# Performance work log

Hardware: AMD Instinct MI355X
Metric: run time of the kernel (lower is better)

The kernel has to match this reference:

```python
import jax, jax.numpy as jnp
import numpy as np
import math

D_MODEL = 1024
D_STATE = 16
D_CONV = 4
EXPAND = 2
D_INNER = EXPAND * D_MODEL
DT_RANK = math.ceil(D_MODEL / 16)
EPS = 1e-5


def setup_inputs() -> dict:
    key = jax.random.key(0)
    ks = jax.random.split(key, 8)
    B, L = 2, 1024
    s = 0.02
    return {
        "hidden_states": jax.random.normal(ks[0], (B, L, D_MODEL), jnp.float32),
        "norm_weight": jnp.ones((D_MODEL,), jnp.float32),
        "in_proj_w": (jax.random.normal(ks[1], (2 * D_INNER, D_MODEL), jnp.float32) * s),
        "conv_w": (jax.random.normal(ks[2], (D_INNER, D_CONV), jnp.float32) * s),
        "conv_b": jnp.zeros((D_INNER,), jnp.float32),
        "x_proj_w": (jax.random.normal(ks[3], (DT_RANK + 2 * D_STATE, D_INNER), jnp.float32) * s),
        "dt_proj_w": (jax.random.normal(ks[4], (D_INNER, DT_RANK), jnp.float32) * s),
        "dt_proj_b": jax.random.uniform(ks[5], (D_INNER,), jnp.float32, -4.0, -2.0),
        "A_log": jnp.log(jnp.broadcast_to(jnp.arange(1, D_STATE + 1, dtype=jnp.float32), (D_INNER, D_STATE))),
        "D": jnp.ones((D_INNER,), jnp.float32),
        "out_proj_w": (jax.random.normal(ks[6], (D_MODEL, D_INNER), jnp.float32) * s),
    }


def _rmsnorm(x, w):
    # Faithful to source: rms = ||x||_2 / sqrt(d); x / (rms + eps) * w
    norm = jnp.linalg.norm(x, axis=-1, keepdims=True)
    rms = norm * (1.0 / math.sqrt(x.shape[-1]))
    return w * (x / (rms + EPS))


def _mamba(h, in_proj_w, conv_w, conv_b, x_proj_w, dt_proj_w, dt_proj_b, A_log, D, out_proj_w):
    B, L, _ = h.shape
    xz = h @ in_proj_w.T                      # (B,L,2*D_INNER)
    x, z = jnp.split(xz, 2, axis=-1)          # each (B,L,D_INNER)

    # causal depthwise conv1d along L, kernel D_CONV
    xpad = jnp.pad(x, ((0, 0), (D_CONV - 1, 0), (0, 0)))
    xc = conv_b
    for k in range(D_CONV):                   # tiny fixed loop over kernel taps
        xc = xc + xpad[:, k:k + L, :] * conv_w[:, k]
    xc = jax.nn.silu(xc)                      # (B,L,D_INNER)

    x_dbl = xc @ x_proj_w.T                   # (B,L,DT_RANK+2N)
    dt, Bm, Cm = jnp.split(x_dbl, [DT_RANK, DT_RANK + D_STATE], axis=-1)
    dt = jax.nn.softplus(dt @ dt_proj_w.T + dt_proj_b)   # (B,L,D_INNER)

    A = -jnp.exp(A_log)                       # (D_INNER,N)
    deltaA = jnp.exp(dt[..., None] * A)                      # (B,L,D_INNER,N)
    deltaBu = (dt * xc)[..., None] * Bm[:, :, None, :]        # (B,L,D_INNER,N)

    def step(hst, inp):
        dA, dBu, Ct = inp
        hst = dA * hst + dBu                  # (B,D_INNER,N)
        y = jnp.einsum('bdn,bn->bd', hst, Ct)
        return hst, y

    h0 = jnp.zeros((B, D_INNER, D_STATE), xc.dtype)
    _, ys = jax.lax.scan(step, h0, (deltaA.swapaxes(0, 1), deltaBu.swapaxes(0, 1), Cm.swapaxes(0, 1)))
    y = ys.swapaxes(0, 1)                     # (B,L,D_INNER)
    y = y + D * xc
    y = y * jax.nn.silu(z)
    return y @ out_proj_w.T                   # (B,L,D_MODEL)


def reference(hidden_states, norm_weight, in_proj_w, conv_w, conv_b, x_proj_w,
              dt_proj_w, dt_proj_b, A_log, D, out_proj_w):
    residual = hidden_states
    h = _rmsnorm(residual, norm_weight)
    out = _mamba(h, in_proj_w, conv_w, conv_b, x_proj_w, dt_proj_w, dt_proj_b,
                 A_log, D, out_proj_w)
    return out, residual
```

## Files before the change

### kernel.cpp

```cpp
#include <hip/hip_runtime.h>

typedef __bf16 bf16x8 __attribute__((ext_vector_type(8)));
typedef float f32x4 __attribute__((ext_vector_type(4)));

__device__ __forceinline__ float b2f(ushort u) {
    union { unsigned int i; float f; } v;
    v.i = ((unsigned int)u) << 16;
    return v.f;
}
__device__ __forceinline__ ushort f2b(float f) {
    union { float f; unsigned int i; } v;
    v.f = f;
    unsigned int x = v.i;
    unsigned int r = (x + 0x7fffu + ((x >> 16) & 1u)) >> 16;
    return (ushort)r;
}
__device__ __forceinline__ float fexp2(float x) {
#if __has_builtin(__builtin_amdgcn_exp2f)
    return __builtin_amdgcn_exp2f(x);
#else
    return exp2f(x);
#endif
}
__device__ __forceinline__ void gload16(const ushort* g, ushort* l) {
    __builtin_amdgcn_global_load_lds(
        (const __attribute__((address_space(1))) unsigned int*)g,
        (__attribute__((address_space(3))) unsigned int*)l, 16, 0, 0);
}
__device__ __forceinline__ bf16x8 ldsfrag(const ushort* s, int row, int cq) {
    int p = cq ^ (row & 7);
    return *(const bf16x8*)(s + row * 64 + p * 8);
}

#define D_MODEL 1024
#define D_INNER 2048
#define D_STATE 16
#define DT_RANK 64
#define NTOK    2048
#define LSEQ    1024
#define NCH     32
#define LC      32
#define KSL     16
#define LOG2E   1.44269504088896f

__global__ __launch_bounds__(256) void prep_kernel(
    const float* __restrict__ hs, const float* __restrict__ w,
    ushort* __restrict__ hout, float* __restrict__ resid,
    const float* __restrict__ inproj, const float* __restrict__ outproj,
    const float* __restrict__ xprojw, const float* __restrict__ dtw,
    ushort* __restrict__ wIn, ushort* __restrict__ wOut,
    ushort* __restrict__ xpw, ushort* __restrict__ dtwb,
    float* __restrict__ xdbl, float* __restrict__ outz)
{
    int blk = blockIdx.x;
    int tid = threadIdx.x;
    if (blk < NTOK) {
        int t = blk;
        float4 r4 = *(const float4*)(hs + (size_t)t * D_MODEL + tid * 4);
        float s = r4.x * r4.x + r4.y * r4.y + r4.z * r4.z + r4.w * r4.w;
        #pragma unroll
        for (int off = 32; off >= 1; off >>= 1) s += __shfl_xor(s, off);
        __shared__ float red[4];
        int lane = tid & 63, wid = tid >> 6;
        if (lane == 0) red[wid] = s;
        __syncthreads();
        float tot = red[0] + red[1] + red[2] + red[3];
        float inv = 1.0f / (sqrtf(tot) * (1.0f / 32.0f) + 1e-5f);
        float4 w4 = *(const float4*)(w + tid * 4);
        ushort4 o;
        o.x = f2b(w4.x * r4.x * inv);
        o.y = f2b(w4.y * r4.y * inv);
        o.z = f2b(w4.z * r4.z * inv);
        o.w = f2b(w4.w * r4.w * inv);
        *(ushort4*)(hout + (size_t)t * D_MODEL + tid * 4) = o;
        *(float4*)(resid + (size_t)t * D_MODEL + tid * 4) = r4;
    } else if (blk < NTOK + 6464) {
        int i = (blk - NTOK) * 256 + tid;
        const float* src; ushort* dst; int off;
        if (i < 1048576)      { src = inproj;  dst = wIn;  off = i; }
        else if (i < 1572864) { src = outproj; dst = wOut; off = i - 1048576; }
        else if (i < 1622016) { src = xprojw;  dst = xpw;  off = i - 1572864; }
        else if (i < 1654784) { src = dtw;     dst = dtwb; off = i - 1622016; }
        else return;
        float4 v = *(const float4*)(src + (size_t)off * 4);
        ushort4 o;
        o.x = f2b(v.x); o.y = f2b(v.y); o.z = f2b(v.z); o.w = f2b(v.w);
        *(ushort4*)(dst + (size_t)off * 4) = o;
    } else if (blk < NTOK + 6464 + 192) {
        int i = (blk - NTOK - 6464) * 256 + tid;
        if (i < 49152)
            *(float4*)(xdbl + (size_t)i * 4) = (float4){0.f, 0.f, 0.f, 0.f};
    } else {
        int i = (blk - NTOK - 6464 - 192) * 256 + tid;
        if (i < 524288)
            *(float4*)(outz + (size_t)i * 4) = (float4){0.f, 0.f, 0.f, 0.f};
    }
}

__global__ __launch_bounds__(256) void gemm_xz_kernel(
    const ushort* __restrict__ Ag, const ushort* __restrict__ Wg,
    ushort* __restrict__ xq, ushort* __restrict__ zq, int K)
{
    __shared__ __align__(16) ushort sA[128 * 64];
    __shared__ __align__(16) ushort sB[128 * 64];
    int tid = threadIdx.x;
    int bm = blockIdx.x, bn = blockIdx.y;
    int wid = tid >> 6, lane = tid & 63;
    int wm = (wid >> 1) * 64, wn = (wid & 1) * 64;
    int l16 = lane & 15, q = lane >> 4;

    f32x4 acc[4][4];
    #pragma unroll
    for (int i = 0; i < 4; i++)
        #pragma unroll
        for (int j = 0; j < 4; j++)
            acc[i][j] = (f32x4){0.f, 0.f, 0.f, 0.f};

    const ushort* Abase = Ag + (size_t)bm * 128 * K;
    const ushort* Wbase = Wg + (size_t)bn * 128 * K;

    int segr = lane >> 3, segc = lane & 7;
    size_t goff[4]; int sseg[4];
    #pragma unroll
    for (int t = 0; t < 4; t++) {
        int s = wid * 4 + t;
        int r = s * 8 + segr;
        int gc = segc ^ (r & 7);
        sseg[t] = s * 512;
        goff[t] = (size_t)r * K + gc * 8;
    }

    for (int k0 = 0; k0 < K; k0 += 64) {
        __syncthreads();
        #pragma unroll
        for (int t = 0; t < 4; t++) {
            gload16(Abase + goff[t] + k0, sA + sseg[t]);
            gload16(Wbase + goff[t] + k0, sB + sseg[t]);
        }
        __syncthreads();
        #pragma unroll
        for (int ks = 0; ks < 2; ks++) {
            int cq = ks * 4 + q;
            bf16x8 af[4], bfr[4];
            #pragma unroll
            for (int i = 0; i < 4; i++)
                af[i] = ldsfrag(sA, wm + i * 16 + l16, cq);
            #pragma unroll
            for (int j = 0; j < 4; j++)
                bfr[j] = ldsfrag(sB, wn + j * 16 + l16, cq);
            #pragma unroll
            for (int i = 0; i < 4; i++)
                #pragma unroll
                for (int j = 0; j < 4; j++)
                    acc[i][j] = __builtin_amdgcn_mfma_f32_16x16x32_bf16(af[i], bfr[j], acc[i][j], 0, 0, 0);
        }
    }

    ushort* dst = (bn < 16) ? xq : zq;
    int row0 = bm * 128 + wm + q * 4;
    int col0 = (bn & 15) * 128 + wn + l16;
    #pragma unroll
    for (int i = 0; i < 4; i++)
        #pragma unroll
        for (int j = 0; j < 4; j++)
            #pragma unroll
            for (int r = 0; r < 4; r++)
                dst[(size_t)(row0 + i * 16 + r) * D_INNER + col0 + j * 16] =
                    f2b(acc[i][j][r]);
}

__global__ __launch_bounds__(256) void gemm_out_kernel(
    const ushort* __restrict__ Ag, const ushort* __restrict__ Wg,
    float* __restrict__ Cf)
{
    __shared__ __align__(16) ushort sA[128 * 64];
    __shared__ __align__(16) ushort sB[128 * 64];
    const int K = D_INNER;
    int tid = threadIdx.x;
    int bm = blockIdx.x, bn = blockIdx.y, bz = blockIdx.z;
    int wid = tid >> 6, lane = tid & 63;
    int wm = (wid >> 1) * 64, wn = (wid & 1) * 64;
    int l16 = lane & 15, q = lane >> 4;

    f32x4 acc[4][4];
    #pragma unroll
    for (int i = 0; i < 4; i++)
        #pragma unroll
        for (int j = 0; j < 4; j++)
            acc[i][j] = (f32x4){0.f, 0.f, 0.f, 0.f};

    const ushort* Abase = Ag + (size_t)bm * 128 * K;
    const ushort* Wbase = Wg + (size_t)bn * 128 * K;

    int segr = lane >> 3, segc = lane & 7;
    size_t goff[4]; int sseg[4];
    #pragma unroll
    for (int t = 0; t < 4; t++) {
        int s = wid * 4 + t;
        int r = s * 8 + segr;
        int gc = segc ^ (r & 7);
        sseg[t] = s * 512;
        goff[t] = (size_t)r * K + gc * 8;
    }

    int kbeg = bz * (K / 2), kend = kbeg + K / 2;
    for (int k0 = kbeg; k0 < kend; k0 += 64) {
        __syncthreads();
        #pragma unroll
        for (int t = 0; t < 4; t++) {
            gload16(Abase + goff[t] + k0, sA + sseg[t]);
            gload16(Wbase + goff[t] + k0, sB + sseg[t]);
        }
        __syncthreads();
        #pragma unroll
        for (int ks = 0; ks < 2; ks++) {
            int cq = ks * 4 + q;
            bf16x8 af[4], bfr[4];
            #pragma unroll
            for (int i = 0; i < 4; i++)
                af[i] = ldsfrag(sA, wm + i * 16 + l16, cq);
            #pragma unroll
            for (int j = 0; j < 4; j++)
                bfr[j] = ldsfrag(sB, wn + j * 16 + l16, cq);
            #pragma unroll
            for (int i = 0; i < 4; i++)
                #pragma unroll
                for (int j = 0; j < 4; j++)
                    acc[i][j] = __builtin_amdgcn_mfma_f32_16x16x32_bf16(af[i], bfr[j], acc[i][j], 0, 0, 0);
        }
    }

    int row0 = bm * 128 + wm + q * 4;
    int col0 = bn * 128 + wn + l16;
    #pragma unroll
    for (int i = 0; i < 4; i++)
        #pragma unroll
        for (int j = 0; j < 4; j++)
            #pragma unroll
            for (int r = 0; r < 4; r++)
                atomicAdd(&Cf[(size_t)(row0 + i * 16 + r) * D_MODEL + col0 + j * 16],
                          acc[i][j][r]);
}

__global__ __launch_bounds__(256) void conv_silu_kernel(
    const ushort* __restrict__ xq, const float* __restrict__ cw,
    const float* __restrict__ cb, ushort* __restrict__ xcb)
{
    int t = blockIdx.x;
    int d0 = threadIdx.x * 8;
    int l = t & (LSEQ - 1), b = t >> 10;

    ushort v[4][8];
    bool has[4];
    #pragma unroll
    for (int k = 0; k < 4; k++) {
        int ll = l - 3 + k;
        has[k] = (ll >= 0);
        if (has[k])
            *(uint4*)v[k] = *(const uint4*)(xq + (((size_t)(b * LSEQ + ll)) << 11) + d0);
    }
    ushort o[8];
    #pragma unroll
    for (int j = 0; j < 8; j++) {
        float4 w4 = *(const float4*)(cw + (size_t)(d0 + j) * 4);
        float wk[4] = {w4.x, w4.y, w4.z, w4.w};
        float acc = cb[d0 + j];
        #pragma unroll
        for (int k = 0; k < 4; k++)
            if (has[k]) acc += b2f(v[k][j]) * wk[k];
        o[j] = f2b(acc / (1.f + __expf(-acc)));
    }
    *(uint4*)(xcb + (((size_t)t) << 11) + d0) = *(const uint4*)o;
}

__global__ __launch_bounds__(256) void xproj_partial_kernel(
    const ushort* __restrict__ xcb, const ushort* __restrict__ wq,
    float* __restrict__ xdbl)
{
    __shared__ __align__(16) ushort sA[128 * 40];
    __shared__ __align__(16) ushort sB[96 * 40];
    int tid = threadIdx.x;
    int bm = blockIdx.x, sl = blockIdx.y;
    int wid = tid >> 6, lane = tid & 63;
    int wm = wid * 32;
    int l16 = lane & 15, q = lane >> 4;

    f32x4 acc[2][6];
    #pragma unroll
    for (int i = 0; i < 2; i++)
        #pragma unroll
        for (int j = 0; j < 6; j++)
            acc[i][j] = (f32x4){0.f, 0.f, 0.f, 0.f};

    const ushort* Abase = xcb + (size_t)bm * 128 * D_INNER;
    int kbase = sl * (D_INNER / KSL);

    for (int kk = 0; kk < D_INNER / KSL; kk += 32) {
        int k0 = kbase + kk;
        __syncthreads();
        #pragma unroll
        for (int i = tid; i < 512; i += 256) {
            int r = i >> 2, c = (i & 3) << 3;
            *(uint4*)(sA + r * 40 + c) = *(const uint4*)(Abase + (size_t)r * D_INNER + k0 + c);
        }
        for (int i = tid; i < 384; i += 256) {
            int r = i >> 2, c = (i & 3) << 3;
            *(uint4*)(sB + r * 40 + c) = *(const uint4*)(wq + (size_t)r * D_INNER + k0 + c);
        }
        __syncthreads();
        bf16x8 af[2], bfr[6];
        #pragma unroll
        for (int i = 0; i < 2; i++)
            af[i] = *(const bf16x8*)(sA + (wm + i * 16 + l16) * 40 + q * 8);
        #pragma unroll
        for (int j = 0; j < 6; j++)
            bfr[j] = *(const bf16x8*)(sB + (j * 16 + l16) * 40 + q * 8);
        #pragma unroll
        for (int i = 0; i < 2; i++)
            #pragma unroll
            for (int j = 0; j < 6; j++)
                acc[i][j] = __builtin_amdgcn_mfma_f32_16x16x32_bf16(af[i], bfr[j], acc[i][j], 0, 0, 0);
    }

    int row0 = bm * 128 + wm + q * 4;
    #pragma unroll
    for (int i = 0; i < 2; i++)
        #pragma unroll
        for (int j = 0; j < 6; j++)
            #pragma unroll
            for (int r = 0; r < 4; r++)
                atomicAdd(&xdbl[(size_t)(row0 + i * 16 + r) * 96 + j * 16 + l16],
                          acc[i][j][r]);
}

__global__ __launch_bounds__(256) void dt_gemm_kernel(
    const float* __restrict__ xdbl, const ushort* __restrict__ dtwq,
    const float* __restrict__ dtb, ushort* __restrict__ dtout)
{
    __shared__ __align__(16) ushort sA[64 * 72];
    __shared__ __align__(16) ushort sB[64 * 72];
    int tid = threadIdx.x;
    int bm = blockIdx.x, bn = blockIdx.y;
    int wid = tid >> 6, lane = tid & 63;
    int wm = wid * 16;
    int l16 = lane & 15, q = lane >> 4;

    const float* Abase = xdbl + (size_t)bm * 64 * 96;
    const ushort* Bbase = dtwq + (size_t)bn * 64 * DT_RANK;
    #pragma unroll
    for (int i = tid; i < 512; i += 256) {
        int r = i >> 3, c = (i & 7) << 3;
        float4 v0 = *(const float4*)(Abase + (size_t)r * 96 + c);
        float4 v1 = *(const float4*)(Abase + (size_t)r * 96 + c + 4);
        ushort o[8] = {f2b(v0.x), f2b(v0.y), f2b(v0.z), f2b(v0.w),
                       f2b(v1.x), f2b(v1.y), f2b(v1.z), f2b(v1.w)};
        *(uint4*)(sA + r * 72 + c) = *(const uint4*)o;
        *(uint4*)(sB + r * 72 + c) = *(const uint4*)(Bbase + (size_t)r * DT_RANK + c);
    }
    __syncthreads();

    f32x4 acc[4];
    #pragma unroll
    for (int j = 0; j < 4; j++) acc[j] = (f32x4){0.f, 0.f, 0.f, 0.f};

    #pragma unroll
    for (int ks = 0; ks < 2; ks++) {
        bf16x8 af = *(const bf16x8*)(sA + (wm + l16) * 72 + ks * 32 + q * 8);
        bf16x8 bfr[4];
        #pragma unroll
        for (int j = 0; j < 4; j++)
            bfr[j] = *(const bf16x8*)(sB + (j * 16 + l16) * 72 + ks * 32 + q * 8);
        #pragma unroll
        for (int j = 0; j < 4; j++)
            acc[j] = __builtin_amdgcn_mfma_f32_16x16x32_bf16(af, bfr[j], acc[j], 0, 0, 0);
    }

    __syncthreads();
    #pragma unroll
    for (int j = 0; j < 4; j++) {
        float bias = dtb[bn * 64 + j * 16 + l16];
        #pragma unroll
        for (int r = 0; r < 4; r++) {
            float s = acc[j][r] + bias;
            float sp = (s > 20.f) ? s : log1pf(__expf(s));
            sA[(wm + q * 4 + r) * 72 + j * 16 + l16] = f2b(sp);
        }
    }
    __syncthreads();
    int row0 = bm * 64, col0 = bn * 64;
    #pragma unroll
    for (int rep = 0; rep < 2; rep++) {
        int off = rep * 2048 + tid * 8;
        int row = off >> 6, col = off & 63;
        *(uint4*)(dtout + (size_t)(row0 + row) * D_INNER + col0 + col) =
            *(const uint4*)(sA + row * 72 + col);
    }
}

__global__ __launch_bounds__(256) void scan_partA_kernel(
    const ushort* __restrict__ dt, const ushort* __restrict__ xcq,
    const float* __restrict__ xdbl, const float* __restrict__ Alog,
    float2* __restrict__ ch)
{
    __shared__ float sBC[LC][32];
    int bid = blockIdx.x;
    int g = bid & 7;
    int c = (bid >> 3) & (NCH - 1);
    int b = bid >> 8;
    int tid = threadIdx.x;
    int lane = tid & 63, wid = tid >> 6;
    int d = g * 256 + wid * 64 + lane;
    int l0 = c * LC;

    {
        int r = tid >> 3, c4 = (tid & 7) * 4;
        *(float4*)&sBC[r][c4] =
            *(const float4*)(xdbl + ((size_t)(b * LSEQ + l0 + r)) * 96 + 64 + c4);
    }
    float A[16];
    #pragma unroll
    for (int k = 0; k < 4; k++)
        *(float4*)&A[k * 4] = *(const float4*)(Alog + d * D_STATE + k * 4);
    #pragma unroll
    for (int n = 0; n < 16; n++) A[n] = -__expf(A[n]) * LOG2E;
    __syncthreads();

    const ushort* dtp = dt  + ((size_t)(b * LSEQ + l0)) * D_INNER + d;
    const ushort* xcp = xcq + ((size_t)(b * LSEQ + l0)) * D_INNER + d;

    float h[16], ap[16];
    #pragma unroll
    for (int n = 0; n < 16; n++) { h[n] = 0.f; ap[n] = 1.f; }

    #pragma unroll 4
    for (int l = 0; l < LC; l++) {
        float dtv = b2f(dtp[(size_t)l * D_INNER]);
        float xcv = b2f(xcp[(size_t)l * D_INNER]);
        float t = dtv * xcv;
        float Bv[16];
        #pragma unroll
        for (int k = 0; k < 4; k++)
            *(float4*)&Bv[k * 4] = *(const float4*)&sBC[l][k * 4];
        #pragma unroll
        for (int n = 0; n < 16; n++) {
            float a = fexp2(dtv * A[n]);
            h[n] = h[n] * a + t * Bv[n];
            ap[n] *= a;
        }
    }

    float2* outp = ch + (((size_t)(c * 2 + b)) << 15) + (d << 4);
    #pragma unroll
    for (int n = 0; n < 16; n += 2) {
        float4 v = {ap[n], h[n], ap[n + 1], h[n + 1]};
        *(float4*)&outp[n] = v;
    }
}

__global__ __launch_bounds__(256) void scan_partB_kernel(
    const float2* __restrict__ ch, float* __restrict__ hinit)
{
    int kk = blockIdx.x * 256 + threadIdx.x;
    int b = kk >> 15, dn = kk & 32767;
    float run = 0.f;
    #pragma unroll 8
    for (int c = 0; c < NCH; c++) {
        size_t off = (((size_t)(c * 2 + b)) << 15) + dn;
        float2 v = ch[off];
        hinit[off] = run;
        run = v.x * run + v.y;
    }
}

__global__ __launch_bounds__(256) void scan_partC_kernel(
    const ushort* __restrict__ dt, const ushort* __restrict__ xcq,
    const float* __restrict__ xdbl, const ushort* __restrict__ zq,
    const float* __restrict__ Alog, const float* __restrict__ Dp,
    const float* __restrict__ hinit, ushort* __restrict__ yg)
{
    __shared__ float sBC[LC][32];
    int bid = blockIdx.x;
    int g = bid & 7;
    int c = (bid >> 3) & (NCH - 1);
    int b = bid >> 8;
    int tid = threadIdx.x;
    int lane = tid & 63, wid = tid >> 6;
    int d = g * 256 + wid * 64 + lane;
    int l0 = c * LC;

    {
        int r = tid >> 3, c4 = (tid & 7) * 4;
        *(float4*)&sBC[r][c4] =
            *(const float4*)(xdbl + ((size_t)(b * LSEQ + l0 + r)) * 96 + 64 + c4);
    }
    float A[16];
    #pragma unroll
    for (int k = 0; k < 4; k++)
        *(float4*)&A[k * 4] = *(const float4*)(Alog + d * D_STATE + k * 4);
    #pragma unroll
    for (int n = 0; n < 16; n++) A[n] = -__expf(A[n]) * LOG2E;
    float Dd = Dp[d];

    const float* hp = hinit + (((size_t)(c * 2 + b)) << 15) + (d << 4);
    float h[16];
    #pragma unroll
    for (int n = 0; n < 16; n += 4)
        *(float4*)&h[n] = *(const float4*)(hp + n);
    __syncthreads();

    const ushort* dtp = dt  + ((size_t)(b * LSEQ + l0)) * D_INNER + d;
    const ushort* xcp = xcq + ((size_t)(b * LSEQ + l0)) * D_INNER + d;
    const ushort* zp  = zq  + ((size_t)(b * LSEQ + l0)) * D_INNER + d;
    ushort* yp = yg + ((size_t)(b * LSEQ + l0)) * D_INNER + d;

    #pragma unroll 4
    for (int l = 0; l < LC; l++) {
        float dtv = b2f(dtp[(size_t)l * D_INNER]);
        float xcv = b2f(xcp[(size_t)l * D_INNER]);
        float zv  = b2f(zp[(size_t)l * D_INNER]);
        float t = dtv * xcv;
        float Bv[16], Cv[16];
        #pragma unroll
        for (int k = 0; k < 4; k++) {
            *(float4*)&Bv[k * 4] = *(const float4*)&sBC[l][k * 4];
            *(float4*)&Cv[k * 4] = *(const float4*)&sBC[l][16 + k * 4];
        }
        float p0 = 0.f, p1 = 0.f, p2 = 0.f, p3 = 0.f;
        #pragma unroll
        for (int n = 0; n < 16; n += 4) {
            float a0 = fexp2(dtv * A[n]);
            float a1 = fexp2(dtv * A[n + 1]);
            float a2 = fexp2(dtv * A[n + 2]);
            float a3 = fexp2(dtv * A[n + 3]);
            h[n]     = h[n] * a0 + t * Bv[n];
            h[n + 1] = h[n + 1] * a1 + t * Bv[n + 1];
            h[n + 2] = h[n + 2] * a2 + t * Bv[n + 2];
            h[n + 3] = h[n + 3] * a3 + t * Bv[n + 3];
            p0 += h[n] * Cv[n];
            p1 += h[n + 1] * Cv[n + 1];
            p2 += h[n + 2] * Cv[n + 2];
            p3 += h[n + 3] * Cv[n + 3];
        }
        float p = (p0 + p1) + (p2 + p3);
        float y = p + Dd * xcv;
        float sz = zv / (1.f + __expf(-zv));
        yp[(size_t)l * D_INNER] = f2b(y * sz);
    }
}

extern "C" void kernel_launch(void* const* d_in, const int* in_sizes, int n_in,
                              void* d_out, int out_size, void* d_ws, size_t ws_size,
                              hipStream_t stream)
{
    const float* hs      = (const float*)d_in[0];
    const float* norm_w  = (const float*)d_in[1];
    const float* inproj  = (const float*)d_in[2];
    const float* convw   = (const float*)d_in[3];
    const float* convb   = (const float*)d_in[4];
    const float* xprojw  = (const float*)d_in[5];
    const float* dtw     = (const float*)d_in[6];
    const float* dtb     = (const float*)d_in[7];
    const float* alog    = (const float*)d_in[8];
    const float* dvec    = (const float*)d_in[9];
    const float* outproj = (const float*)d_in[10];

    float* out_main  = (float*)d_out;
    float* out_resid = (float*)d_out + (size_t)NTOK * D_MODEL;

    char* ws = (char*)d_ws;
    ushort* xq      = (ushort*)(ws);
    ushort* zq      = (ushort*)(ws +  8388608);
    ushort* dtq     = (ushort*)(ws + 16777216);
    ushort* xcb     = (ushort*)(ws + 25165824);
    float2* ch      = (float2*)(ws + 33554432);
    float*  hinit   = (float*) (ws + 50331648);
    float*  xdbl    = (float*) (ws + 67108864);
    ushort* wIn     = (ushort*)(ws + 67895296);
    ushort* wOut    = (ushort*)(ws + 76283904);
    ushort* h_bf16  = (ushort*)(ws + 80478208);
    ushort* xpw_b   = (ushort*)(ws + 84672512);
    ushort* dtw_b   = (ushort*)(ws + 85065728);
    ushort* yg_bf16 = (ushort*)(ws + 85327872);

    prep_kernel<<<NTOK + 6464 + 192 + 2048, 256, 0, stream>>>(
        hs, norm_w, h_bf16, out_resid,
        inproj, outproj, xprojw, dtw, wIn, wOut, xpw_b, dtw_b, xdbl, out_main);

    gemm_xz_kernel<<<dim3(NTOK / 128, (2 * D_INNER) / 128), 256, 0, stream>>>(
        h_bf16, wIn, xq, zq, D_MODEL);

    conv_silu_kernel<<<NTOK, 256, 0, stream>>>(xq, convw, convb, xcb);

    xproj_partial_kernel<<<dim3(NTOK / 128, KSL), 256, 0, stream>>>(
        xcb, xpw_b, xdbl);

    dt_gemm_kernel<<<dim3(NTOK / 64, D_INNER / 64), 256, 0, stream>>>(
        xdbl, dtw_b, dtb, dtq);

    scan_partA_kernel<<<512, 256, 0, stream>>>(dtq, xcb, xdbl, alog, ch);
    scan_partB_kernel<<<256, 256, 0, stream>>>(ch, hinit);
    scan_partC_kernel<<<512, 256, 0, stream>>>(dtq, xcb, xdbl, zq,
                                               alog, dvec, hinit, yg_bf16);

    gemm_out_kernel<<<dim3(NTOK / 128, D_MODEL / 128, 2), 256, 0, stream>>>(
        yg_bf16, wOut, out_main);
}
```

Measured before the change: 277.8 us.

## Replace split-K atomic output GEMM with 64x64 tile direct-store GEMM

The output projection GEMM moves from 128x128 tiles with split-K=2 and float atomicAdd to 64x64 tiles over the full K, storing results directly. This removes the atomics and the zero-fill of the output buffer in the prep kernel. The grid grows from 256 to 512 blocks for better CU coverage, at the cost of lower per-block data reuse. The scan kernels also drop their explicit unroll-4 pragmas.

```diff
diff --git a/kernel.cpp b/kernel.cpp
--- a/kernel.cpp
+++ b/kernel.cpp
@@ -50,7 +50,7 @@
     const float* __restrict__ xprojw, const float* __restrict__ dtw,
     ushort* __restrict__ wIn, ushort* __restrict__ wOut,
     ushort* __restrict__ xpw, ushort* __restrict__ dtwb,
-    float* __restrict__ xdbl, float* __restrict__ outz)
+    float* __restrict__ xdbl)
 {
     int blk = blockIdx.x;
     int tid = threadIdx.x;
@@ -86,14 +86,10 @@
         ushort4 o;
         o.x = f2b(v.x); o.y = f2b(v.y); o.z = f2b(v.z); o.w = f2b(v.w);
         *(ushort4*)(dst + (size_t)off * 4) = o;
-    } else if (blk < NTOK + 6464 + 192) {
+    } else {
         int i = (blk - NTOK - 6464) * 256 + tid;
         if (i < 49152)
             *(float4*)(xdbl + (size_t)i * 4) = (float4){0.f, 0.f, 0.f, 0.f};
-    } else {
-        int i = (blk - NTOK - 6464 - 192) * 256 + tid;
-        if (i < 524288)
-            *(float4*)(outz + (size_t)i * 4) = (float4){0.f, 0.f, 0.f, 0.f};
     }
 }
 
@@ -169,45 +165,40 @@
                     f2b(acc[i][j][r]);
 }
 
-__global__ __launch_bounds__(256) void gemm_out_kernel(
+__global__ __launch_bounds__(256) void gemm64_kernel(
     const ushort* __restrict__ Ag, const ushort* __restrict__ Wg,
-    float* __restrict__ Cf)
-{
-    __shared__ __align__(16) ushort sA[128 * 64];
-    __shared__ __align__(16) ushort sB[128 * 64];
-    const int K = D_INNER;
-    int tid = threadIdx.x;
-    int bm = blockIdx.x, bn = blockIdx.y, bz = blockIdx.z;
+    float* __restrict__ Cf, int M, int N, int K)
+{
+    __shared__ __align__(16) ushort sA[64 * 64];
+    __shared__ __align__(16) ushort sB[64 * 64];
+    int tid = threadIdx.x;
+    int bm = blockIdx.x, bn = blockIdx.y;
     int wid = tid >> 6, lane = tid & 63;
-    int wm = (wid >> 1) * 64, wn = (wid & 1) * 64;
+    int wm = wid * 16;
     int l16 = lane & 15, q = lane >> 4;
 
-    f32x4 acc[4][4];
-    #pragma unroll
-    for (int i = 0; i < 4; i++)
-        #pragma unroll
-        for (int j = 0; j < 4; j++)
-            acc[i][j] = (f32x4){0.f, 0.f, 0.f, 0.f};
-
-    const ushort* Abase = Ag + (size_t)bm * 128 * K;
-    const ushort* Wbase = Wg + (size_t)bn * 128 * K;
+    f32x4 acc[4];
+    #pragma unroll
+    for (int j = 0; j < 4; j++) acc[j] = (f32x4){0.f, 0.f, 0.f, 0.f};
+
+    const ushort* Abase = Ag + (size_t)bm * 64 * K;
+    const ushort* Wbase = Wg + (size_t)bn * 64 * K;
 
     int segr = lane >> 3, segc = lane & 7;
-    size_t goff[4]; int sseg[4];
-    #pragma unroll
-    for (int t = 0; t < 4; t++) {
-        int s = wid * 4 + t;
+    size_t goff[2]; int sseg[2];
+    #pragma unroll
+    for (int t = 0; t < 2; t++) {
+        int s = wid * 2 + t;
         int r = s * 8 + segr;
         int gc = segc ^ (r & 7);
         sseg[t] = s * 512;
         goff[t] = (size_t)r * K + gc * 8;
     }
 
-    int kbeg = bz * (K / 2), kend = kbeg + K / 2;
-    for (int k0 = kbeg; k0 < kend; k0 += 64) {
-        __syncthreads();
-        #pragma unroll
-        for (int t = 0; t < 4; t++) {
+    for (int k0 = 0; k0 < K; k0 += 64) {
+        __syncthreads();
+        #pragma unroll
+        for (int t = 0; t < 2; t++) {
             gload16(Abase + goff[t] + k0, sA + sseg[t]);
             gload16(Wbase + goff[t] + k0, sB + sseg[t]);
         }
@@ -215,31 +206,24 @@
         #pragma unroll
         for (int ks = 0; ks < 2; ks++) {
             int cq = ks * 4 + q;
-            bf16x8 af[4], bfr[4];
-            #pragma unroll
-            for (int i = 0; i < 4; i++)
-                af[i] = ldsfrag(sA, wm + i * 16 + l16, cq);
+            bf16x8 af = ldsfrag(sA, wm + l16, cq);
+            bf16x8 bfr[4];
             #pragma unroll
             for (int j = 0; j < 4; j++)
-                bfr[j] = ldsfrag(sB, wn + j * 16 + l16, cq);
-            #pragma unroll
-            for (int i = 0; i < 4; i++)
-                #pragma unroll
-                for (int j = 0; j < 4; j++)
-                    acc[i][j] = __builtin_amdgcn_mfma_f32_16x16x32_bf16(af[i], bfr[j], acc[i][j], 0, 0, 0);
-        }
-    }
-
-    int row0 = bm * 128 + wm + q * 4;
-    int col0 = bn * 128 + wn + l16;
-    #pragma unroll
-    for (int i = 0; i < 4; i++)
-        #pragma unroll
-        for (int j = 0; j < 4; j++)
-            #pragma unroll
-            for (int r = 0; r < 4; r++)
-                atomicAdd(&Cf[(size_t)(row0 + i * 16 + r) * D_MODEL + col0 + j * 16],
-                          acc[i][j][r]);
+                bfr[j] = ldsfrag(sB, j * 16 + l16, cq);
+            #pragma unroll
+            for (int j = 0; j < 4; j++)
+                acc[j] = __builtin_amdgcn_mfma_f32_16x16x32_bf16(af, bfr[j], acc[j], 0, 0, 0);
+        }
+    }
+
+    int row0 = bm * 64 + wm + q * 4;
+    int col0 = bn * 64 + l16;
+    #pragma unroll
+    for (int j = 0; j < 4; j++)
+        #pragma unroll
+        for (int r = 0; r < 4; r++)
+            Cf[(size_t)(row0 + r) * N + col0 + j * 16] = acc[j][r];
 }
 
 __global__ __launch_bounds__(256) void conv_silu_kernel(
@@ -432,7 +416,6 @@
     #pragma unroll
     for (int n = 0; n < 16; n++) { h[n] = 0.f; ap[n] = 1.f; }
 
-    #pragma unroll 4
     for (int l = 0; l < LC; l++) {
         float dtv = b2f(dtp[(size_t)l * D_INNER]);
         float xcv = b2f(xcp[(size_t)l * D_INNER]);
@@ -513,7 +496,6 @@
     const ushort* zp  = zq  + ((size_t)(b * LSEQ + l0)) * D_INNER + d;
     ushort* yp = yg + ((size_t)(b * LSEQ + l0)) * D_INNER + d;
 
-    #pragma unroll 4
     for (int l = 0; l < LC; l++) {
         float dtv = b2f(dtp[(size_t)l * D_INNER]);
         float xcv = b2f(xcp[(size_t)l * D_INNER]);
@@ -582,9 +564,9 @@
     ushort* dtw_b   = (ushort*)(ws + 85065728);
     ushort* yg_bf16 = (ushort*)(ws + 85327872);
 
-    prep_kernel<<<NTOK + 6464 + 192 + 2048, 256, 0, stream>>>(
+    prep_kernel<<<NTOK + 6464 + 192, 256, 0, stream>>>(
         hs, norm_w, h_bf16, out_resid,
-        inproj, outproj, xprojw, dtw, wIn, wOut, xpw_b, dtw_b, xdbl, out_main);
+        inproj, outproj, xprojw, dtw, wIn, wOut, xpw_b, dtw_b, xdbl);
 
     gemm_xz_kernel<<<dim3(NTOK / 128, (2 * D_INNER) / 128), 256, 0, stream>>>(
         h_bf16, wIn, xq, zq, D_MODEL);
@@ -602,6 +584,6 @@
     scan_partC_kernel<<<512, 256, 0, stream>>>(dtq, xcb, xdbl, zq,
                                                alog, dvec, hinit, yg_bf16);
 
-    gemm_out_kernel<<<dim3(NTOK / 128, D_MODEL / 128, 2), 256, 0, stream>>>(
-        yg_bf16, wOut, out_main);
-}
+    gemm64_kernel<<<dim3(NTOK / 64, D_MODEL / 64), 256, 0, stream>>>(
+        yg_bf16, wOut, out_main, NTOK, D_MODEL, D_INNER);
+}
```

After: 262.9 us. 1.06x faster.
